# Performance work log

Measured on AMD Instinct MI355X. Metric: run time of the kernel, lower is better.

## Reference

```python
import jax, jax.numpy as jnp
import numpy as np

B, S, D = 2, 2048, 1024
H, DH = 16, 64  # num_heads, hidden_dimension (per-head)


def setup_inputs() -> dict:
    key = jax.random.key(0)
    ks = jax.random.split(key, 9)
    s = 1.0 / np.sqrt(D)
    so = 1.0 / np.sqrt(H * DH)
    return {
        "x": jax.random.normal(ks[0], (B, S, D), dtype=jnp.float32),
        "Wq": jax.random.uniform(ks[1], (D, H * DH), jnp.float32, -s, s),
        "bq": jax.random.uniform(ks[2], (H * DH,), jnp.float32, -s, s),
        "Wk": jax.random.uniform(ks[3], (D, H * DH), jnp.float32, -s, s),
        "bk": jax.random.uniform(ks[4], (H * DH,), jnp.float32, -s, s),
        "Wv": jax.random.uniform(ks[5], (D, H * DH), jnp.float32, -s, s),
        "bv": jax.random.uniform(ks[6], (H * DH,), jnp.float32, -s, s),
        "Wo": jax.random.uniform(ks[7], (H * DH, D), jnp.float32, -so, so),
        "bo": jax.random.uniform(ks[8], (D,), jnp.float32, -so, so),
    }


def reference(x, Wq, bq, Wk, bk, Wv, bv, Wo, bo):
    b, s, _ = x.shape
    # project and split heads: [b, h, s, dh]
    q = (x @ Wq + bq).reshape(b, s, H, DH).transpose(0, 2, 1, 3)
    k = (x @ Wk + bk).reshape(b, s, H, DH).transpose(0, 2, 1, 3)
    v = (x @ Wv + bv).reshape(b, s, H, DH).transpose(0, 2, 1, 3)
    scores = jnp.einsum('bhqd,bhkd->bhqk', q, k) / jnp.sqrt(jnp.float32(DH))
    causal = jnp.triu(jnp.ones((s, s), dtype=bool), k=1)
    scores = jnp.where(causal, -jnp.inf, scores)
    weights = jax.nn.softmax(scores, axis=-1)
    out = jnp.einsum('bhqk,bhkd->bhqd', weights, v)
    out = out.transpose(0, 2, 1, 3).reshape(b, s, H * DH)
    return out @ Wo + bo
```

## Files before the change

### kernel.cpp

```cpp
#include <hip/hip_runtime.h>

#define B_  2
#define S_  2048
#define D_  1024
#define H_  16
#define DH_ 64
#define NDH (H_*DH_)
#define BS_ (B_*S_)
#define PER ((size_t)B_*H_*S_*DH_)

typedef __bf16 bf16;
typedef bf16 bf16x8 __attribute__((ext_vector_type(8)));
typedef bf16 bf16x4 __attribute__((ext_vector_type(4)));
typedef float f32x4 __attribute__((ext_vector_type(4)));

#define QSCALE 0.18033688011112042f

#define AS1 __attribute__((address_space(1)))
#define AS3 __attribute__((address_space(3)))
__device__ inline void gld16(const bf16* g, bf16* l) {
    __builtin_amdgcn_global_load_lds((const AS1 void*)g, (AS3 void*)l, 16, 0, 0);
}

__global__ __launch_bounds__(256) void prep(
        const float* __restrict__ x,
        const float* __restrict__ W0, const float* __restrict__ W1,
        const float* __restrict__ W2, const float* __restrict__ W3,
        bf16* __restrict__ xb, bf16* __restrict__ T0, bf16* __restrict__ T1,
        bf16* __restrict__ T2, bf16* __restrict__ T3) {
    __shared__ float T[32][33];
    int bid = blockIdx.x, t = threadIdx.x;
    if (bid < 4096) {
        int i = (bid * 256 + t) * 4;
        float4 v = *(const float4*)(x + i);
        bf16x4 o = { (bf16)v.x, (bf16)v.y, (bf16)v.z, (bf16)v.w };
        *(bf16x4*)(xb + i) = o;
        return;
    }
    int r2 = bid - 4096;
    int z = r2 >> 10, w = r2 & 1023;
    const float* W = (z == 0) ? W0 : (z == 1) ? W1 : (z == 2) ? W2 : W3;
    bf16* Wt = (z == 0) ? T0 : (z == 1) ? T1 : (z == 2) ? T2 : T3;
    int k0 = (w >> 5) * 32, n0 = (w & 31) * 32;
    int r = t >> 3, c = (t & 7) * 4;
    float4 v = *(const float4*)(W + (size_t)(k0 + r) * 1024 + n0 + c);
    T[c + 0][r] = v.x; T[c + 1][r] = v.y; T[c + 2][r] = v.z; T[c + 3][r] = v.w;
    __syncthreads();
    bf16x4 o = { (bf16)T[r][c], (bf16)T[r][c + 1], (bf16)T[r][c + 2], (bf16)T[r][c + 3] };
    *(bf16x4*)(Wt + (size_t)(n0 + r) * 1024 + k0 + c) = o;
}

__global__ __launch_bounds__(256) void qkv_gemm(
        const bf16* __restrict__ A, const bf16* __restrict__ Bt,
        const float* __restrict__ bq, const float* __restrict__ bk,
        const float* __restrict__ bv, bf16* __restrict__ Qout, bf16* __restrict__ Vt) {
    __shared__ __align__(16) bf16 As[3][128 * 32];
    __shared__ __align__(16) bf16 Bs[3][128 * 32];
    int tid = threadIdx.x, wave = tid >> 6, lane = tid & 63;
    int quad = lane >> 4, l16 = lane & 15;

    int flat = blockIdx.y * 24 + blockIdx.x;
    int swz  = (flat & 7) * 96 + (flat >> 3);
    int bm = (swz / 24) * 128, bn = (swz % 24) * 128;
    int wm = (wave >> 1) * 64, wn = (wave & 1) * 64;

    int sr = lane >> 2;
    int sc = (((lane & 3) ^ ((sr ^ (sr >> 2)) & 3)) * 8);
    const bf16* Ag0 = A + (size_t)(bm + (wave * 2 + 0) * 16 + sr) * 1024 + sc;
    const bf16* Ag1 = A + (size_t)(bm + (wave * 2 + 1) * 16 + sr) * 1024 + sc;
    const bf16* Bg0 = Bt + (size_t)(bn + (wave * 2 + 0) * 16 + sr) * 1024 + sc;
    const bf16* Bg1 = Bt + (size_t)(bn + (wave * 2 + 1) * 16 + sr) * 1024 + sc;
    int la0 = (wave * 2 + 0) * 512;
    int la1 = (wave * 2 + 1) * 512;

    int rsw = (l16 ^ (l16 >> 2)) & 3;

    f32x4 acc[4][4] = {};

    auto stage = [&](int buf, int t) {
        int k0 = t * 32;
        gld16(Ag0 + k0, &As[buf][la0]);
        gld16(Ag1 + k0, &As[buf][la1]);
        gld16(Bg0 + k0, &Bs[buf][la0]);
        gld16(Bg1 + k0, &Bs[buf][la1]);
    };

    stage(0, 0);
    stage(1, 1);

    for (int t = 0; t < 32; ++t) {
        if (t < 30) asm volatile("s_waitcnt vmcnt(4)" ::: "memory");
        else        asm volatile("s_waitcnt vmcnt(0)" ::: "memory");
        __builtin_amdgcn_s_barrier();
        if (t + 2 < 32) stage((t + 2) % 3, t + 2);
        int cur = t % 3;
        bf16x8 af[4], bfr[4];
        #pragma unroll
        for (int i = 0; i < 4; ++i)
            af[i] = *(const bf16x8*)&As[cur][(wm + i * 16 + l16) * 32 + (quad ^ rsw) * 8];
        #pragma unroll
        for (int j = 0; j < 4; ++j)
            bfr[j] = *(const bf16x8*)&Bs[cur][(wn + j * 16 + l16) * 32 + (quad ^ rsw) * 8];
        #pragma unroll
        for (int i = 0; i < 4; ++i)
          #pragma unroll
          for (int j = 0; j < 4; ++j)
            acc[i][j] = __builtin_amdgcn_mfma_f32_16x16x32_bf16(af[i], bfr[j], acc[i][j], 0, 0, 0);
    }
    __builtin_amdgcn_s_barrier();

    #pragma unroll
    for (int i = 0; i < 4; ++i)
      #pragma unroll
      for (int j = 0; j < 4; ++j) {
        int col = bn + wn + j * 16 + l16;
        float bias = (col < 1024) ? bq[col] : (col < 2048) ? bk[col - 1024] : bv[col - 2048];
        int qkv = col >> 10, cw = col & 1023;
        int hh = cw >> 6, d = cw & 63;
        int row0 = bm + wm + i * 16 + quad * 4;
        int bb = row0 >> 11, s0 = row0 & 2047;
        if (qkv < 2) {
            float scl = (qkv == 0) ? QSCALE : 1.0f;
            #pragma unroll
            for (int r = 0; r < 4; ++r)
                Qout[(size_t)qkv * PER + (((size_t)bb * H_ + hh) * S_ + s0 + r) * DH_ + d] =
                    (bf16)((acc[i][j][r] + bias) * scl);
        } else {
            bf16x4 pack;
            #pragma unroll
            for (int r = 0; r < 4; ++r) pack[r] = (bf16)(acc[i][j][r] + bias);
            *(bf16x4*)&Vt[(((size_t)bb * H_ + hh) * DH_ + d) * S_ + s0] = pack;
        }
      }
}

__global__ __launch_bounds__(256) void gemm_proj(
        const bf16* __restrict__ A, const bf16* __restrict__ Bt,
        const float* __restrict__ bias, float* __restrict__ out) {
    __shared__ __align__(16) bf16 As[3][128 * 32];
    __shared__ __align__(16) bf16 Bs[3][64 * 32];
    int tid = threadIdx.x, wave = tid >> 6, lane = tid & 63;
    int quad = lane >> 4, l16 = lane & 15;

    int flat = blockIdx.y * 16 + blockIdx.x;
    int swz  = (flat & 7) * 64 + (flat >> 3);
    int bm = (swz / 16) * 128, bn = (swz % 16) * 64;
    int wm = (wave >> 1) * 64, wn = (wave & 1) * 32;

    int sr = lane >> 2;
    int sc = (((lane & 3) ^ ((sr ^ (sr >> 2)) & 3)) * 8);
    const bf16* Ag0 = A + (size_t)(bm + (wave * 2 + 0) * 16 + sr) * 1024 + sc;
    const bf16* Ag1 = A + (size_t)(bm + (wave * 2 + 1) * 16 + sr) * 1024 + sc;
    const bf16* Bg0 = Bt + (size_t)(bn + wave * 16 + sr) * 1024 + sc;
    int la0 = (wave * 2 + 0) * 512;
    int la1 = (wave * 2 + 1) * 512;
    int lb0 = wave * 512;

    int rsw = (l16 ^ (l16 >> 2)) & 3;

    f32x4 acc[4][2] = {};

    auto stage = [&](int buf, int t) {
        int k0 = t * 32;
        gld16(Ag0 + k0, &As[buf][la0]);
        gld16(Ag1 + k0, &As[buf][la1]);
        gld16(Bg0 + k0, &Bs[buf][lb0]);
    };

    stage(0, 0);
    stage(1, 1);

    for (int t = 0; t < 32; ++t) {
        if (t < 30) asm volatile("s_waitcnt vmcnt(3)" ::: "memory");
        else        asm volatile("s_waitcnt vmcnt(0)" ::: "memory");
        __builtin_amdgcn_s_barrier();
        if (t + 2 < 32) stage((t + 2) % 3, t + 2);
        int cur = t % 3;
        bf16x8 af[4], bfr[2];
        #pragma unroll
        for (int i = 0; i < 4; ++i)
            af[i] = *(const bf16x8*)&As[cur][(wm + i * 16 + l16) * 32 + (quad ^ rsw) * 8];
        #pragma unroll
        for (int j = 0; j < 2; ++j)
            bfr[j] = *(const bf16x8*)&Bs[cur][(wn + j * 16 + l16) * 32 + (quad ^ rsw) * 8];
        #pragma unroll
        for (int i = 0; i < 4; ++i)
          #pragma unroll
          for (int j = 0; j < 2; ++j)
            acc[i][j] = __builtin_amdgcn_mfma_f32_16x16x32_bf16(af[i], bfr[j], acc[i][j], 0, 0, 0);
    }
    __builtin_amdgcn_s_barrier();

    #pragma unroll
    for (int i = 0; i < 4; ++i)
      #pragma unroll
      for (int j = 0; j < 2; ++j) {
        int col = bn + wn + j * 16 + l16;
        float b = bias[col];
        #pragma unroll
        for (int r = 0; r < 4; ++r) {
            int row = bm + wm + i * 16 + quad * 4 + r;
            out[(size_t)row * 1024 + col] = acc[i][j][r] + b;
        }
      }
}

__global__ __launch_bounds__(256) void flash15(
        const bf16* __restrict__ Q, const bf16* __restrict__ K,
        const bf16* __restrict__ Vt, bf16* __restrict__ O) {
    int bh = blockIdx.x;
    int b = bh >> 4, h = bh & 15;
    int t = 31 - blockIdx.y;
    int q0 = t * 64;
    int nkt = t + 1;
    int tid = threadIdx.x;
    int wave = tid >> 6, lane = tid & 63;
    int quad = lane >> 4, l16 = lane & 15;
    int lm = l16 & 7;

    __shared__ __align__(16) bf16 Kl[2][64 * 64];
    __shared__ __align__(16) bf16 Vl[2][64 * 64];
    __shared__ bf16 P[4][16][72];

    const bf16* Qb = Q + (size_t)bh * S_ * DH_;
    const bf16* Kb = K + (size_t)bh * S_ * DH_;
    const bf16* Vb = Vt + (size_t)bh * DH_ * S_;

    bf16x8 qf[2];
    {
        const bf16* qp = Qb + (size_t)(q0 + wave * 16 + l16) * DH_ + quad * 8;
        qf[0] = *(const bf16x8*)(qp);
        qf[1] = *(const bf16x8*)(qp + 32);
    }

    bf16x8 ones;
    #pragma unroll
    for (int j = 0; j < 8; ++j) ones[j] = (l16 == 0) ? (bf16)1.0f : (bf16)0.0f;

    f32x4 oacc[4] = {};
    f32x4 lacc = {};

    int r8 = lane >> 3, c8 = lane & 7;
    int sco = ((c8 ^ r8) * 8);

    auto stage = [&](int buf, int kt) {
        int kv0 = kt * 64;
        #pragma unroll
        for (int g = 0; g < 2; ++g) {
            int row = wave * 16 + g * 8;
            gld16(Kb + (size_t)(kv0 + row + r8) * DH_ + sco, &Kl[buf][row * 64]);
            gld16(Vb + (size_t)(row + r8) * S_ + kv0 + sco,   &Vl[buf][row * 64]);
        }
    };

    stage(0, 0);
    __syncthreads();

    for (int kt = 0; kt < nkt; ++kt) {
        int buf = kt & 1;
        if (kt + 1 < nkt) stage(buf ^ 1, kt + 1);
        int kv0 = kt * 64;

        bf16x8 kf[4][2];
        #pragma unroll
        for (int ns = 0; ns < 4; ++ns) {
            int row = ns * 16 + l16;
            kf[ns][0] = *(const bf16x8*)&Kl[buf][row * 64 + ((quad)     ^ lm) * 8];
            kf[ns][1] = *(const bf16x8*)&Kl[buf][row * 64 + ((4 + quad) ^ lm) * 8];
        }

        f32x4 sacc[4] = {};
        #pragma unroll
        for (int ns = 0; ns < 4; ++ns) {
            sacc[ns] = __builtin_amdgcn_mfma_f32_16x16x32_bf16(kf[ns][0], qf[0], sacc[ns], 0, 0, 0);
            sacc[ns] = __builtin_amdgcn_mfma_f32_16x16x32_bf16(kf[ns][1], qf[1], sacc[ns], 0, 0, 0);
        }

        bool diag = (kt == nkt - 1);
        #pragma unroll
        for (int ns = 0; ns < 4; ++ns) {
            bf16x4 pk;
            #pragma unroll
            for (int r = 0; r < 4; ++r) {
                float p = __builtin_amdgcn_exp2f(sacc[ns][r]);
                if (diag) {
                    int kv = kv0 + ns * 16 + quad * 4 + r;
                    int qq = q0 + wave * 16 + l16;
                    if (kv > qq) p = 0.f;
                }
                pk[r] = (bf16)p;
            }
            *(bf16x4*)&P[wave][l16][ns * 16 + quad * 4] = pk;
        }

        #pragma unroll
        for (int ks = 0; ks < 2; ++ks) {
            bf16x8 pf = *(const bf16x8*)&P[wave][l16][ks * 32 + quad * 8];
            lacc = __builtin_amdgcn_mfma_f32_16x16x32_bf16(pf, ones, lacc, 0, 0, 0);
            #pragma unroll
            for (int ds = 0; ds < 4; ++ds) {
                bf16x8 vf = *(const bf16x8*)&Vl[buf][(ds * 16 + l16) * 64 + ((ks * 4 + quad) ^ lm) * 8];
                oacc[ds] = __builtin_amdgcn_mfma_f32_16x16x32_bf16(pf, vf, oacc[ds], 0, 0, 0);
            }
        }

        __syncthreads();
    }

    float ls[4];
    #pragma unroll
    for (int r = 0; r < 4; ++r) ls[r] = __shfl(lacc[r], quad << 4);
    #pragma unroll
    for (int ds = 0; ds < 4; ++ds)
      #pragma unroll
      for (int r = 0; r < 4; ++r) {
          int qq = q0 + wave * 16 + quad * 4 + r;
          O[((size_t)b * S_ + qq) * NDH + h * DH_ + ds * 16 + l16] = (bf16)(oacc[ds][r] / ls[r]);
      }
}

extern "C" void kernel_launch(void* const* d_in, const int* in_sizes, int n_in,
                              void* d_out, int out_size, void* d_ws, size_t ws_size,
                              hipStream_t stream) {
    const float* x  = (const float*)d_in[0];
    const float* Wq = (const float*)d_in[1];
    const float* bq = (const float*)d_in[2];
    const float* Wk = (const float*)d_in[3];
    const float* bk = (const float*)d_in[4];
    const float* Wv = (const float*)d_in[5];
    const float* bv = (const float*)d_in[6];
    const float* Wo = (const float*)d_in[7];
    const float* bo = (const float*)d_in[8];
    float* out = (float*)d_out;

    bf16* ws = (bf16*)d_ws;
    const size_t M1 = (size_t)1024 * 1024;
    bf16* xb    = ws;
    bf16* WqkvT = ws + 4 * M1;
    bf16* WoT   = ws + 7 * M1;
    bf16* Qw    = ws + 8 * M1;
    bf16* Vtw   = ws + 16 * M1;
    bf16* Ow    = ws + 20 * M1;

    prep<<<8192, 256, 0, stream>>>(x, Wq, Wk, Wv, Wo,
                                   xb, WqkvT, WqkvT + M1, WqkvT + 2 * M1, WoT);

    qkv_gemm<<<dim3(3072 / 128, BS_ / 128), 256, 0, stream>>>(xb, WqkvT, bq, bk, bv, Qw, Vtw);

    flash15<<<dim3(B_ * H_, 32), 256, 0, stream>>>(Qw, Qw + PER, Vtw, Ow);

    gemm_proj<<<dim3(1024 / 64, BS_ / 128), 256, 0, stream>>>(Ow, WoT, bo, out);
}
```

Before: 181.7 us.

## Enlarge QKV GEMM tiles to 256x256x64 with 8 waves and double buffering

Rewrites the QKV projection GEMM to use 256x256 output tiles with K-step 64, 512 threads (8 waves), and a two-stage LDS double buffer with an XOR swizzle over 8 chunks. Loads for the next stage are interleaved into the compute phases, and MFMA sections are wrapped in raised wave priority. The larger tile raises arithmetic intensity and cuts global reloads. In exchange the grid shrinks to 192 blocks, which may underfill the GPU's CUs, and LDS use rises to 128 KB per block.

New measurement: 195.5 us. 1.08x slower.

```diff
diff --git a/kernel.cpp b/kernel.cpp
--- a/kernel.cpp
+++ b/kernel.cpp
@@ -50,74 +50,98 @@
     *(bf16x4*)(Wt + (size_t)(n0 + r) * 1024 + k0 + c) = o;
 }
 
-__global__ __launch_bounds__(256) void qkv_gemm(
+__global__ __launch_bounds__(512) void qkv_gemm8(
         const bf16* __restrict__ A, const bf16* __restrict__ Bt,
         const float* __restrict__ bq, const float* __restrict__ bk,
         const float* __restrict__ bv, bf16* __restrict__ Qout, bf16* __restrict__ Vt) {
-    __shared__ __align__(16) bf16 As[3][128 * 32];
-    __shared__ __align__(16) bf16 Bs[3][128 * 32];
+    __shared__ __align__(16) bf16 As[2][256 * 64];
+    __shared__ __align__(16) bf16 Bs[2][256 * 64];
     int tid = threadIdx.x, wave = tid >> 6, lane = tid & 63;
-    int quad = lane >> 4, l16 = lane & 15;
-
-    int flat = blockIdx.y * 24 + blockIdx.x;
-    int swz  = (flat & 7) * 96 + (flat >> 3);
-    int bm = (swz / 24) * 128, bn = (swz % 24) * 128;
-    int wm = (wave >> 1) * 64, wn = (wave & 1) * 64;
-
-    int sr = lane >> 2;
-    int sc = (((lane & 3) ^ ((sr ^ (sr >> 2)) & 3)) * 8);
-    const bf16* Ag0 = A + (size_t)(bm + (wave * 2 + 0) * 16 + sr) * 1024 + sc;
-    const bf16* Ag1 = A + (size_t)(bm + (wave * 2 + 1) * 16 + sr) * 1024 + sc;
-    const bf16* Bg0 = Bt + (size_t)(bn + (wave * 2 + 0) * 16 + sr) * 1024 + sc;
-    const bf16* Bg1 = Bt + (size_t)(bn + (wave * 2 + 1) * 16 + sr) * 1024 + sc;
-    int la0 = (wave * 2 + 0) * 512;
-    int la1 = (wave * 2 + 1) * 512;
-
-    int rsw = (l16 ^ (l16 >> 2)) & 3;
-
-    f32x4 acc[4][4] = {};
-
-    auto stage = [&](int buf, int t) {
-        int k0 = t * 32;
-        gld16(Ag0 + k0, &As[buf][la0]);
-        gld16(Ag1 + k0, &As[buf][la1]);
-        gld16(Bg0 + k0, &Bs[buf][la0]);
-        gld16(Bg1 + k0, &Bs[buf][la1]);
+    int quad = lane >> 4, l16 = lane & 15, lm = l16 & 7;
+    int wr = wave >> 2, wc = wave & 3;
+
+    int flat = blockIdx.y * 12 + blockIdx.x;
+    int swz  = (flat & 7) * 24 + (flat >> 3);
+    int bm = (swz / 12) * 256, bn = (swz % 12) * 256;
+
+    int r8 = lane >> 3, c8 = lane & 7;
+    int scx = (c8 ^ r8) * 8;
+
+    const bf16* Agb = A + (size_t)bm * 1024;
+    const bf16* Bgb = Bt + (size_t)bn * 1024;
+
+    f32x4 acc[8][4] = {};
+
+    auto stageA = [&](int b, int kt) {
+        int k0 = kt * 64;
+        #pragma unroll
+        for (int s = 0; s < 4; ++s) {
+            int row = s * 64 + wave * 8;
+            gld16(Agb + (size_t)(row + r8) * 1024 + k0 + scx, &As[b][row * 64]);
+        }
     };
-
-    stage(0, 0);
-    stage(1, 1);
-
-    for (int t = 0; t < 32; ++t) {
-        if (t < 30) asm volatile("s_waitcnt vmcnt(4)" ::: "memory");
-        else        asm volatile("s_waitcnt vmcnt(0)" ::: "memory");
+    auto stageB = [&](int b, int kt) {
+        int k0 = kt * 64;
+        #pragma unroll
+        for (int s = 0; s < 4; ++s) {
+            int row = s * 64 + wave * 8;
+            gld16(Bgb + (size_t)(row + r8) * 1024 + k0 + scx, &Bs[b][row * 64]);
+        }
+    };
+
+    stageA(0, 0); stageB(0, 0);
+    asm volatile("s_waitcnt vmcnt(0)" ::: "memory");
+    __builtin_amdgcn_s_barrier();
+
+    for (int kt = 0; kt < 16; ++kt) {
+        int b = kt & 1;
+        #pragma unroll
+        for (int p = 0; p < 4; ++p) {
+            if (p == 0 && kt + 1 < 16) stageA(b ^ 1, kt + 1);
+            if (p == 1 && kt + 1 < 16) stageB(b ^ 1, kt + 1);
+            const int mh = p >> 1, nh = p & 1;
+
+            bf16x8 af[4][2], bfr[2][2];
+            #pragma unroll
+            for (int i = 0; i < 4; ++i) {
+                int row = wr * 128 + (mh * 4 + i) * 16 + l16;
+                #pragma unroll
+                for (int ks = 0; ks < 2; ++ks)
+                    af[i][ks] = *(const bf16x8*)&As[b][row * 64 + ((ks * 4 + quad) ^ lm) * 8];
+            }
+            #pragma unroll
+            for (int j = 0; j < 2; ++j) {
+                int row = wc * 64 + (nh * 2 + j) * 16 + l16;
+                #pragma unroll
+                for (int ks = 0; ks < 2; ++ks)
+                    bfr[j][ks] = *(const bf16x8*)&Bs[b][row * 64 + ((ks * 4 + quad) ^ lm) * 8];
+            }
+
+            __builtin_amdgcn_s_setprio(1);
+            #pragma unroll
+            for (int i = 0; i < 4; ++i)
+              #pragma unroll
+              for (int j = 0; j < 2; ++j) {
+                acc[mh * 4 + i][nh * 2 + j] = __builtin_amdgcn_mfma_f32_16x16x32_bf16(
+                    af[i][0], bfr[j][0], acc[mh * 4 + i][nh * 2 + j], 0, 0, 0);
+                acc[mh * 4 + i][nh * 2 + j] = __builtin_amdgcn_mfma_f32_16x16x32_bf16(
+                    af[i][1], bfr[j][1], acc[mh * 4 + i][nh * 2 + j], 0, 0, 0);
+              }
+            __builtin_amdgcn_s_setprio(0);
+        }
+        asm volatile("s_waitcnt vmcnt(0)" ::: "memory");
         __builtin_amdgcn_s_barrier();
-        if (t + 2 < 32) stage((t + 2) % 3, t + 2);
-        int cur = t % 3;
-        bf16x8 af[4], bfr[4];
-        #pragma unroll
-        for (int i = 0; i < 4; ++i)
-            af[i] = *(const bf16x8*)&As[cur][(wm + i * 16 + l16) * 32 + (quad ^ rsw) * 8];
-        #pragma unroll
-        for (int j = 0; j < 4; ++j)
-            bfr[j] = *(const bf16x8*)&Bs[cur][(wn + j * 16 + l16) * 32 + (quad ^ rsw) * 8];
-        #pragma unroll
-        for (int i = 0; i < 4; ++i)
-          #pragma unroll
-          for (int j = 0; j < 4; ++j)
-            acc[i][j] = __builtin_amdgcn_mfma_f32_16x16x32_bf16(af[i], bfr[j], acc[i][j], 0, 0, 0);
-    }
-    __builtin_amdgcn_s_barrier();
-
-    #pragma unroll
-    for (int i = 0; i < 4; ++i)
+    }
+
+    #pragma unroll
+    for (int i = 0; i < 8; ++i)
       #pragma unroll
       for (int j = 0; j < 4; ++j) {
-        int col = bn + wn + j * 16 + l16;
+        int col = bn + wc * 64 + j * 16 + l16;
         float bias = (col < 1024) ? bq[col] : (col < 2048) ? bk[col - 1024] : bv[col - 2048];
         int qkv = col >> 10, cw = col & 1023;
         int hh = cw >> 6, d = cw & 63;
-        int row0 = bm + wm + i * 16 + quad * 4;
+        int row0 = bm + wr * 128 + i * 16 + quad * 4;
         int bb = row0 >> 11, s0 = row0 & 2047;
         if (qkv < 2) {
             float scl = (qkv == 0) ? QSCALE : 1.0f;
@@ -345,7 +369,7 @@
     prep<<<8192, 256, 0, stream>>>(x, Wq, Wk, Wv, Wo,
                                    xb, WqkvT, WqkvT + M1, WqkvT + 2 * M1, WoT);
 
-    qkv_gemm<<<dim3(3072 / 128, BS_ / 128), 256, 0, stream>>>(xb, WqkvT, bq, bk, bv, Qw, Vtw);
+    qkv_gemm8<<<dim3(12, 16), 512, 0, stream>>>(xb, WqkvT, bq, bk, bv, Qw, Vtw);
 
     flash15<<<dim3(B_ * H_, 32), 256, 0, stream>>>(Qw, Qw + PER, Vtw, Ow);
 
```
